# Kernel optimization log

Hardware: AMD Instinct MI355X
Metric: run time of the kernel (lower is better)

Reference implementation:

```python
import jax, jax.numpy as jnp
import numpy as np

E = 1024      # hidden_size
H = 16        # num_attention_heads
HD = E // H   # head_dim
EPS = 1e-5


def _mw_linear(x, Wt, bt, Wi, bi, split):
    # multiway linear: text weights on tokens [:split], image weights on [split:]
    xt = x[:, :split] @ Wt.T + bt
    xi = x[:, split:] @ Wi.T + bi
    return jnp.concatenate([xt, xi], axis=1)


def _ln(x, g, b):
    mu = jnp.mean(x, axis=-1, keepdims=True)
    var = jnp.mean(jnp.square(x - mu), axis=-1, keepdims=True)
    return (x - mu) * jax.lax.rsqrt(var + EPS) * g + b


def _mw_ln(x, gt, bt, gi, bi, split):
    return jnp.concatenate([_ln(x[:, :split], gt, bt), _ln(x[:, split:], gi, bi)], axis=1)


def setup_inputs() -> dict:
    key = jax.random.key(0)
    ks = jax.random.split(key, 24)
    B, T = 8, 1024
    d = {
        'query': jax.random.normal(ks[0], (B, T, E), jnp.float32),
        'key': jax.random.normal(ks[1], (B, T, E), jnp.float32),
        'value': jax.random.normal(ks[2], (B, T, E), jnp.float32),
        'attention_mask': jax.random.normal(ks[3], (T, T), jnp.float32) * 0.02,
    }
    i = 4
    for name in ['q', 'k', 'v', 'o']:
        d[f'W{name}_t'] = jax.random.normal(ks[i], (E, E), jnp.float32) * 0.02; i += 1
        d[f'b{name}_t'] = jnp.zeros((E,), jnp.float32)
        d[f'W{name}_i'] = jax.random.normal(ks[i], (E, E), jnp.float32) * 0.02; i += 1
        d[f'b{name}_i'] = jnp.zeros((E,), jnp.float32)
    d['ln_g_t'] = jnp.ones((E,), jnp.float32)
    d['ln_b_t'] = jnp.zeros((E,), jnp.float32)
    d['ln_g_i'] = jnp.ones((E,), jnp.float32)
    d['ln_b_i'] = jnp.zeros((E,), jnp.float32)
    d['split_position'] = 64
    return d


def reference(query, key, value, attention_mask,
              Wq_t, bq_t, Wq_i, bq_i,
              Wk_t, bk_t, Wk_i, bk_i,
              Wv_t, bv_t, Wv_i, bv_i,
              Wo_t, bo_t, Wo_i, bo_i,
              ln_g_t, ln_b_t, ln_g_i, ln_b_i,
              split_position):
    B, T, _ = query.shape
    S = key.shape[1]
    scaling = HD ** -0.5
    q = _mw_linear(query, Wq_t, bq_t, Wq_i, bq_i, split_position) * scaling
    k = _mw_linear(key, Wk_t, bk_t, Wk_i, bk_i, split_position)
    v = _mw_linear(value, Wv_t, bv_t, Wv_i, bv_i, split_position)
    q = q.reshape(B, T, H, HD)
    k = k.reshape(B, S, H, HD)
    v = v.reshape(B, S, H, HD)
    # [B, H, T, S] attention logits
    attn_weights = jnp.einsum('bthd,bshd->bhts', q, k)
    attn_weights = jnp.nan_to_num(attn_weights) + attention_mask[None, None]
    probs = jax.nn.softmax(attn_weights.astype(jnp.float32), axis=-1).astype(attn_weights.dtype)
    attn = jnp.einsum('bhts,bshd->bthd', probs, v).reshape(B, T, E)
    attn = _mw_ln(attn, ln_g_t, ln_b_t, ln_g_i, ln_b_i, split_position)
    attn = _mw_linear(attn, Wo_t, bo_t, Wo_i, bo_i, split_position)
    return attn
```

## Files before the change

### kernel.cpp

```cpp
#include <hip/hip_runtime.h>

#define E_DIM 1024
#define HEADS 16
#define HD 64

typedef unsigned short ushort_t;
typedef __attribute__((ext_vector_type(8))) short bf16x8;
typedef __attribute__((ext_vector_type(4))) float floatx4;

__device__ inline unsigned int pack2bf(float a, float b) {
    unsigned int ua = __builtin_bit_cast(unsigned int, a);
    unsigned int ub = __builtin_bit_cast(unsigned int, b);
    ua = (ua + 0x8000u) >> 16;
    ub = (ub + 0x8000u) & 0xFFFF0000u;
    return ua | ub;
}
__device__ inline unsigned short f2bf(float a) {
    return (unsigned short)((__builtin_bit_cast(unsigned int, a) + 0x8000u) >> 16);
}
__device__ inline float bf2f(unsigned int s) {
    return __builtin_bit_cast(float, s << 16);
}

__device__ __forceinline__ void load_lds16(const void* g, void* l) {
    __builtin_amdgcn_global_load_lds(
        (const __attribute__((address_space(1))) unsigned int*)g,
        (__attribute__((address_space(3))) unsigned int*)l, 16, 0, 0);
}

__global__ __launch_bounds__(256) void cvt_f32_bf16(
    const float* __restrict__ in, ushort_t* __restrict__ out)
{
    size_t i = ((size_t)blockIdx.x * 256 + threadIdx.x) * 8;
    float4 a = *(const float4*)&in[i];
    float4 b = *(const float4*)&in[i + 4];
    uint4 o;
    o.x = pack2bf(a.x, a.y); o.y = pack2bf(a.z, a.w);
    o.z = pack2bf(b.x, b.y); o.w = pack2bf(b.z, b.w);
    *(uint4*)&out[i] = o;
}

__global__ __launch_bounds__(256) void cvt_weights(
    const float* w0, const float* w1, const float* w2, const float* w3,
    const float* w4, const float* w5, const float* w6, const float* w7,
    ushort_t* __restrict__ out)
{
    const float* srcs[8] = {w0, w1, w2, w3, w4, w5, w6, w7};
    const float* __restrict__ src = srcs[blockIdx.y];
    ushort_t* __restrict__ dst = out + (size_t)blockIdx.y * E_DIM * E_DIM;
    size_t i = ((size_t)blockIdx.x * 256 + threadIdx.x) * 8;
    float4 a = *(const float4*)&src[i];
    float4 b = *(const float4*)&src[i + 4];
    uint4 o;
    o.x = pack2bf(a.x, a.y); o.y = pack2bf(a.z, a.w);
    o.z = pack2bf(b.x, b.y); o.w = pack2bf(b.z, b.w);
    *(uint4*)&dst[i] = o;
}

template<bool OUT_BF16>
__global__ __launch_bounds__(256) void gemm_mw(
    const ushort_t* __restrict__ x,
    const ushort_t* __restrict__ Wt,
    const float* __restrict__ bt,
    const ushort_t* __restrict__ Wi,
    const float* __restrict__ bi,
    void* __restrict__ outv,
    const int* __restrict__ split_ptr,
    float scale, int T_)
{
    const int split = *split_ptr;
    const int kind = blockIdx.z;
    const int m0 = blockIdx.y * 128;
    const int n0 = blockIdx.x * 128;
    const int t0 = m0 % T_;

    if (kind == 0) { if (t0 >= split) return; }
    else           { if (t0 + 128 <= split) return; }

    const ushort_t* __restrict__ W    = (kind == 0) ? Wt : Wi;
    const float*    __restrict__ bias = (kind == 0) ? bt : bi;

    __shared__ __align__(16) ushort_t As[128 * 32];
    __shared__ __align__(16) ushort_t Bs[128 * 32];

    const int tid  = threadIdx.x;
    const int lane = tid & 63;
    const int wv   = tid >> 6;
    const int rw   = (wv >> 1) * 64;
    const int cw   = (wv & 1) * 64;
    const int am   = lane & 15;
    const int aq   = lane >> 4;

    const int grow = wv * 32 + (lane >> 2);
    const int gcol = (lane & 3) * 8;

    floatx4 acc[4][4];
    #pragma unroll
    for (int i = 0; i < 4; ++i)
        #pragma unroll
        for (int j = 0; j < 4; ++j)
            acc[i][j] = (floatx4){0.f, 0.f, 0.f, 0.f};

    for (int k0 = 0; k0 < E_DIM; k0 += 32) {
        load_lds16(&x[(size_t)(m0 + grow) * E_DIM + k0 + gcol],      &As[(wv * 32) * 32]);
        load_lds16(&x[(size_t)(m0 + grow + 16) * E_DIM + k0 + gcol], &As[(wv * 32 + 16) * 32]);
        load_lds16(&W[(size_t)(n0 + grow) * E_DIM + k0 + gcol],      &Bs[(wv * 32) * 32]);
        load_lds16(&W[(size_t)(n0 + grow + 16) * E_DIM + k0 + gcol], &Bs[(wv * 32 + 16) * 32]);
        __syncthreads();

        bf16x8 af[4], bfv[4];
        #pragma unroll
        for (int i = 0; i < 4; ++i)
            af[i] = *(const bf16x8*)&As[(rw + i * 16 + am) * 32 + aq * 8];
        #pragma unroll
        for (int j = 0; j < 4; ++j)
            bfv[j] = *(const bf16x8*)&Bs[(cw + j * 16 + am) * 32 + aq * 8];

        #pragma unroll
        for (int i = 0; i < 4; ++i)
            #pragma unroll
            for (int j = 0; j < 4; ++j)
                acc[i][j] = __builtin_amdgcn_mfma_f32_16x16x32_bf16(af[i], bfv[j], acc[i][j], 0, 0, 0);
        __syncthreads();
    }

    const int cq = lane >> 4;
    const int cm = lane & 15;
    #pragma unroll
    for (int j = 0; j < 4; ++j) {
        int n = n0 + cw + j * 16 + cm;
        float bv = bias[n];
        #pragma unroll
        for (int i = 0; i < 4; ++i) {
            int mbase = m0 + rw + i * 16 + cq * 4;
            #pragma unroll
            for (int r = 0; r < 4; ++r) {
                int m = mbase + r;
                int t = m % T_;
                if (((t < split) ? 0 : 1) != kind) continue;
                float val = (acc[i][j][r] + bv) * scale;
                if (OUT_BF16) ((ushort_t*)outv)[(size_t)m * E_DIM + n] = f2bf(val);
                else          ((float*)outv)[(size_t)m * E_DIM + n] = val;
            }
        }
    }
}

__global__ __launch_bounds__(256) void attn_mfma(
    const ushort_t* __restrict__ q, const ushort_t* __restrict__ k,
    const ushort_t* __restrict__ v, const float* __restrict__ mask,
    ushort_t* __restrict__ outp, int T_)
{
    const int tid  = threadIdx.x;
    const int lane = tid & 63;
    const int wv   = tid >> 6;
    const int h    = blockIdx.y;
    const int b    = blockIdx.z;
    const int r0   = blockIdx.x * 64;

    __shared__ __align__(16) unsigned short Qs[2 * 64 * 40];
    __shared__ __align__(16) unsigned short Ks[2 * 64 * 40];
    __shared__ __align__(16) unsigned short Vst[2 * 64 * 40];
    __shared__ __align__(16) unsigned short Ps[4 * 2 * 16 * 40];

    const int m    = lane & 15;
    const int kq   = lane >> 4;
    const int wrow = wv * 16;

    #pragma unroll
    for (int i = 0; i < 4; ++i) {
        int f   = tid + 256 * i;
        int row = f >> 4;
        int c4  = (f & 15) * 4;
        uint2 a2 = *(const uint2*)&q[((size_t)(b * T_ + r0 + row)) * E_DIM + h * HD + c4];
        int ad = (c4 >> 5) * 2560 + row * 40 + (c4 & 31);
        *(unsigned int*)&Qs[ad]     = a2.x;
        *(unsigned int*)&Qs[ad + 2] = a2.y;
    }
    __syncthreads();

    bf16x8 aq[2];
    aq[0] = *(const bf16x8*)&Qs[0 * 2560 + (wrow + m) * 40 + kq * 8];
    aq[1] = *(const bf16x8*)&Qs[1 * 2560 + (wrow + m) * 40 + kq * 8];

    floatx4 oa[4];
    #pragma unroll
    for (int j = 0; j < 4; ++j) oa[j] = (floatx4){0.f, 0.f, 0.f, 0.f};
    float mrun[4] = {-3.0e38f, -3.0e38f, -3.0e38f, -3.0e38f};
    float lsum[4] = {0.f, 0.f, 0.f, 0.f};

    const int vs0 = (tid >> 4) * 4;
    const int vd0 = (tid & 15) * 4;

    #pragma unroll 1
    for (int s0 = 0; s0 < T_; s0 += 64) {
        __syncthreads();

        #pragma unroll
        for (int i = 0; i < 4; ++i) {
            int f   = tid + 256 * i;
            int row = f >> 4;
            int c4  = (f & 15) * 4;
            uint2 a2 = *(const uint2*)&k[((size_t)(b * T_ + s0 + row)) * E_DIM + h * HD + c4];
            int ad = (c4 >> 5) * 2560 + row * 40 + (c4 & 31);
            *(unsigned int*)&Ks[ad]     = a2.x;
            *(unsigned int*)&Ks[ad + 2] = a2.y;
        }

        {
            uint2 vvr[4];
            #pragma unroll
            for (int i = 0; i < 4; ++i)
                vvr[i] = *(const uint2*)&v[((size_t)(b * T_ + s0 + vs0 + i)) * E_DIM + h * HD + vd0];
            const ushort_t* vp = (const ushort_t*)vvr;
            int plane = (vs0 >> 5) * 2560;
            int sin   = vs0 & 31;
            #pragma unroll
            for (int t = 0; t < 4; ++t) {
                int d  = vd0 + t;
                int pr = d ^ ((d >> 4) & 3);
                uint2 w;
                w.x = (unsigned int)vp[0 * 4 + t] | ((unsigned int)vp[1 * 4 + t] << 16);
                w.y = (unsigned int)vp[2 * 4 + t] | ((unsigned int)vp[3 * 4 + t] << 16);
                *(uint2*)&Vst[plane + pr * 40 + sin] = w;
            }
        }

        float mv[4][4];
        {
            const float* mbase = &mask[(size_t)(r0 + wrow + kq * 4) * T_ + s0 + m];
            #pragma unroll
            for (int j = 0; j < 4; ++j)
                #pragma unroll
                for (int r = 0; r < 4; ++r)
                    mv[j][r] = mbase[r * T_ + j * 16];
        }

        __syncthreads();

        floatx4 sa[4];
        #pragma unroll
        for (int j = 0; j < 4; ++j) sa[j] = (floatx4){0.f, 0.f, 0.f, 0.f};
        #pragma unroll
        for (int c = 0; c < 2; ++c) {
            #pragma unroll
            for (int j = 0; j < 4; ++j) {
                bf16x8 bk = *(const bf16x8*)&Ks[c * 2560 + (j * 16 + m) * 40 + kq * 8];
                sa[j] = __builtin_amdgcn_mfma_f32_16x16x32_bf16(aq[c], bk, sa[j], 0, 0, 0);
            }
        }

        float mnew[4], alpha[4];
        #pragma unroll
        for (int r = 0; r < 4; ++r) {
            sa[0][r] += mv[0][r]; sa[1][r] += mv[1][r];
            sa[2][r] += mv[2][r]; sa[3][r] += mv[3][r];
            float mt = fmaxf(fmaxf(sa[0][r], sa[1][r]), fmaxf(sa[2][r], sa[3][r]));
            mt = fmaxf(mt, __shfl_xor(mt, 1));
            mt = fmaxf(mt, __shfl_xor(mt, 2));
            mt = fmaxf(mt, __shfl_xor(mt, 4));
            mt = fmaxf(mt, __shfl_xor(mt, 8));
            float mn = fmaxf(mrun[r], mt);
            alpha[r] = __expf(mrun[r] - mn);
            mnew[r] = mn;
            mrun[r] = mn;
        }
        #pragma unroll
        for (int j = 0; j < 4; ++j)
            #pragma unroll
            for (int r = 0; r < 4; ++r)
                oa[j][r] *= alpha[r];

        float rs[4] = {0.f, 0.f, 0.f, 0.f};
        #pragma unroll
        for (int j = 0; j < 4; ++j) {
            int gl = ((((j & 1) << 1) | (m >> 3)) ^ kq) & 3;
            int pbase = wv * 1280 + (j >> 1) * 640 + (kq * 4) * 40 + gl * 8 + (m & 7);
            #pragma unroll
            for (int r = 0; r < 4; ++r) {
                float p = __expf(sa[j][r] - mnew[r]);
                rs[r] += p;
                Ps[pbase + r * 40] = f2bf(p);
            }
        }
        #pragma unroll
        for (int r = 0; r < 4; ++r) {
            float s = rs[r];
            s += __shfl_xor(s, 1); s += __shfl_xor(s, 2);
            s += __shfl_xor(s, 4); s += __shfl_xor(s, 8);
            lsum[r] = lsum[r] * alpha[r] + s;
        }

        #pragma unroll
        for (int c = 0; c < 2; ++c) {
            bf16x8 ap = *(const bf16x8*)&Ps[wv * 1280 + c * 640 + m * 40 + ((kq ^ (m >> 2)) & 3) * 8];
            #pragma unroll
            for (int j = 0; j < 4; ++j) {
                int pr = 16 * j + (m ^ j);
                bf16x8 bv = *(const bf16x8*)&Vst[c * 2560 + pr * 40 + kq * 8];
                oa[j] = __builtin_amdgcn_mfma_f32_16x16x32_bf16(ap, bv, oa[j], 0, 0, 0);
            }
        }
    }

    #pragma unroll
    for (int r = 0; r < 4; ++r) {
        float inv = 1.0f / lsum[r];
        size_t orow = ((size_t)(b * T_ + r0 + wrow + kq * 4 + r)) * E_DIM + h * HD;
        #pragma unroll
        for (int j = 0; j < 4; ++j)
            outp[orow + j * 16 + m] = f2bf(oa[j][r] * inv);
    }
}

__global__ __launch_bounds__(256) void mw_ln_bf16(
    const ushort_t* __restrict__ x,
    const float* __restrict__ gt, const float* __restrict__ bt,
    const float* __restrict__ gi, const float* __restrict__ bi,
    ushort_t* __restrict__ out,
    const int* __restrict__ split_ptr, int T_)
{
    const int split = *split_ptr;
    const int row = blockIdx.x;
    const int t = row % T_;
    const float* __restrict__ g  = (t < split) ? gt : gi;
    const float* __restrict__ bb = (t < split) ? bt : bi;

    const int tid = threadIdx.x;
    const int lane = tid & 63;
    const int wid = tid >> 6;

    __shared__ float red[8];

    uint2 xv = *(const uint2*)&x[(size_t)row * E_DIM + tid * 4];
    float f0 = bf2f(xv.x & 0xffffu), f1 = bf2f(xv.x >> 16);
    float f2 = bf2f(xv.y & 0xffffu), f3 = bf2f(xv.y >> 16);
    float s = f0 + f1 + f2 + f3;
    #pragma unroll
    for (int off = 1; off < 64; off <<= 1) s += __shfl_xor(s, off, 64);
    if (lane == 0) red[wid] = s;
    __syncthreads();
    float mu = (red[0] + red[1] + red[2] + red[3]) * (1.0f / E_DIM);

    float d0 = f0 - mu, d1 = f1 - mu, d2 = f2 - mu, d3 = f3 - mu;
    float s2 = d0*d0 + d1*d1 + d2*d2 + d3*d3;
    #pragma unroll
    for (int off = 1; off < 64; off <<= 1) s2 += __shfl_xor(s2, off, 64);
    if (lane == 0) red[4 + wid] = s2;
    __syncthreads();
    float var = (red[4] + red[5] + red[6] + red[7]) * (1.0f / E_DIM);
    float rstd = rsqrtf(var + 1e-5f);

    float4 gv = *(const float4*)&g[tid * 4];
    float4 bv = *(const float4*)&bb[tid * 4];
    uint2 ov;
    ov.x = pack2bf(d0 * rstd * gv.x + bv.x, d1 * rstd * gv.y + bv.y);
    ov.y = pack2bf(d2 * rstd * gv.z + bv.z, d3 * rstd * gv.w + bv.w);
    *(uint2*)&out[(size_t)row * E_DIM + tid * 4] = ov;
}

extern "C" void kernel_launch(void* const* d_in, const int* in_sizes, int n_in,
                              void* d_out, int out_size, void* d_ws, size_t ws_size,
                              hipStream_t stream) {
    const float* query = (const float*)d_in[0];
    const float* key   = (const float*)d_in[1];
    const float* value = (const float*)d_in[2];
    const float* mask  = (const float*)d_in[3];
    const float* Wq_t = (const float*)d_in[4];  const float* bq_t = (const float*)d_in[5];
    const float* Wq_i = (const float*)d_in[6];  const float* bq_i = (const float*)d_in[7];
    const float* Wk_t = (const float*)d_in[8];  const float* bk_t = (const float*)d_in[9];
    const float* Wk_i = (const float*)d_in[10]; const float* bk_i = (const float*)d_in[11];
    const float* Wv_t = (const float*)d_in[12]; const float* bv_t = (const float*)d_in[13];
    const float* Wv_i = (const float*)d_in[14]; const float* bv_i = (const float*)d_in[15];
    const float* Wo_t = (const float*)d_in[16]; const float* bo_t = (const float*)d_in[17];
    const float* Wo_i = (const float*)d_in[18]; const float* bo_i = (const float*)d_in[19];
    const float* ln_g_t = (const float*)d_in[20]; const float* ln_b_t = (const float*)d_in[21];
    const float* ln_g_i = (const float*)d_in[22]; const float* ln_b_i = (const float*)d_in[23];
    const int* split = (const int*)d_in[24];

    float* out = (float*)d_out;

    const int BT = in_sizes[0] / E_DIM;
    const int T_ = 1024;
    const int B  = BT / T_;

    ushort_t* ws = (ushort_t*)d_ws;
    const size_t nx = (size_t)BT * E_DIM;
    const size_t nw = (size_t)E_DIM * E_DIM;
    ushort_t* x_bf = ws;
    ushort_t* q_bf = ws + nx;
    ushort_t* k_bf = ws + 2 * nx;
    ushort_t* v_bf = ws + 3 * nx;
    ushort_t* w_bf = ws + 4 * nx;

    dim3 blk(256);
    dim3 ggrid(E_DIM / 128, BT / 128, 2);
    dim3 agrid(T_ / 64, HEADS, B);
    const int cvt_blocks = (int)(nx / 2048);
    const int wcvt_blocks = (int)(nw / 2048);
    const float scaling = 0.125f;

    cvt_weights<<<dim3(wcvt_blocks, 8), blk, 0, stream>>>(
        Wq_t, Wq_i, Wk_t, Wk_i, Wv_t, Wv_i, Wo_t, Wo_i, w_bf);

    cvt_f32_bf16<<<cvt_blocks, blk, 0, stream>>>(query, x_bf);
    gemm_mw<true><<<ggrid, blk, 0, stream>>>(x_bf, w_bf + 0 * nw, bq_t, w_bf + 1 * nw, bq_i,
                                             q_bf, split, scaling, T_);
    cvt_f32_bf16<<<cvt_blocks, blk, 0, stream>>>(key, x_bf);
    gemm_mw<true><<<ggrid, blk, 0, stream>>>(x_bf, w_bf + 2 * nw, bk_t, w_bf + 3 * nw, bk_i,
                                             k_bf, split, 1.0f, T_);
    cvt_f32_bf16<<<cvt_blocks, blk, 0, stream>>>(value, x_bf);
    gemm_mw<true><<<ggrid, blk, 0, stream>>>(x_bf, w_bf + 4 * nw, bv_t, w_bf + 5 * nw, bv_i,
                                             v_bf, split, 1.0f, T_);

    attn_mfma<<<agrid, blk, 0, stream>>>(q_bf, k_bf, v_bf, mask, q_bf, T_);

    mw_ln_bf16<<<dim3(BT), blk, 0, stream>>>(q_bf, ln_g_t, ln_b_t, ln_g_i, ln_b_i, x_bf, split, T_);

    gemm_mw<false><<<ggrid, blk, 0, stream>>>(x_bf, w_bf + 6 * nw, bo_t, w_bf + 7 * nw, bo_i,
                                              out, split, 1.0f, T_);
}
```

Baseline: 524.0 us.

## Batch QKV projections into one launch and widen attention query tile

The three input conversions now run as a single launch, and the three QKV multiway GEMMs run as one 6-slice grid through a shared GEMM core. The attention kernel now handles 128 query rows per block, two 64-row sub-tiles per wave, so each K/V tile loaded into LDS serves twice as many queries. This cuts launch count and halves K/V global and LDS-staging traffic. In exchange it raises register pressure, halves the attention grid, uses an extra workspace buffer, and places the bf16 Q buffer in the output allocation.

After: 503.2 us. -4.0%, faster.

```diff
diff --git a/kernel.cpp b/kernel.cpp
--- a/kernel.cpp
+++ b/kernel.cpp
@@ -28,16 +28,19 @@
         (__attribute__((address_space(3))) unsigned int*)l, 16, 0, 0);
 }
 
-__global__ __launch_bounds__(256) void cvt_f32_bf16(
-    const float* __restrict__ in, ushort_t* __restrict__ out)
-{
+__global__ __launch_bounds__(256) void cvt_inputs(
+    const float* s0, const float* s1, const float* s2,
+    ushort_t* d0, ushort_t* d1, ushort_t* d2)
+{
+    const float* __restrict__ src = (blockIdx.y == 0) ? s0 : (blockIdx.y == 1) ? s1 : s2;
+    ushort_t* __restrict__ dst = (blockIdx.y == 0) ? d0 : (blockIdx.y == 1) ? d1 : d2;
     size_t i = ((size_t)blockIdx.x * 256 + threadIdx.x) * 8;
-    float4 a = *(const float4*)&in[i];
-    float4 b = *(const float4*)&in[i + 4];
+    float4 a = *(const float4*)&src[i];
+    float4 b = *(const float4*)&src[i + 4];
     uint4 o;
     o.x = pack2bf(a.x, a.y); o.y = pack2bf(a.z, a.w);
     o.z = pack2bf(b.x, b.y); o.w = pack2bf(b.z, b.w);
-    *(uint4*)&out[i] = o;
+    *(uint4*)&dst[i] = o;
 }
 
 __global__ __launch_bounds__(256) void cvt_weights(
@@ -58,28 +61,11 @@
 }
 
 template<bool OUT_BF16>
-__global__ __launch_bounds__(256) void gemm_mw(
-    const ushort_t* __restrict__ x,
-    const ushort_t* __restrict__ Wt,
-    const float* __restrict__ bt,
-    const ushort_t* __restrict__ Wi,
-    const float* __restrict__ bi,
-    void* __restrict__ outv,
-    const int* __restrict__ split_ptr,
-    float scale, int T_)
-{
-    const int split = *split_ptr;
-    const int kind = blockIdx.z;
-    const int m0 = blockIdx.y * 128;
-    const int n0 = blockIdx.x * 128;
-    const int t0 = m0 % T_;
-
-    if (kind == 0) { if (t0 >= split) return; }
-    else           { if (t0 + 128 <= split) return; }
-
-    const ushort_t* __restrict__ W    = (kind == 0) ? Wt : Wi;
-    const float*    __restrict__ bias = (kind == 0) ? bt : bi;
-
+__device__ __forceinline__ void gemm_core(
+    const ushort_t* __restrict__ x, const ushort_t* __restrict__ W,
+    const float* __restrict__ bias, void* __restrict__ outv,
+    int m0, int n0, int split, int kind, float scale, int T_)
+{
     __shared__ __align__(16) ushort_t As[128 * 32];
     __shared__ __align__(16) ushort_t Bs[128 * 32];
 
@@ -146,7 +132,54 @@
     }
 }
 
-__global__ __launch_bounds__(256) void attn_mfma(
+__global__ __launch_bounds__(256) void gemm_qkv(
+    const ushort_t* __restrict__ xq, const ushort_t* __restrict__ xk,
+    const ushort_t* __restrict__ xv, const ushort_t* __restrict__ wall,
+    const float* bq_t, const float* bq_i, const float* bk_t, const float* bk_i,
+    const float* bv_t, const float* bv_i,
+    ushort_t* oq, ushort_t* ok, ushort_t* ov,
+    const int* __restrict__ split_ptr, int T_)
+{
+    const int split = *split_ptr;
+    const int z = blockIdx.z;
+    const int op = z >> 1;
+    const int kind = z & 1;
+    const int m0 = blockIdx.y * 128;
+    const int n0 = blockIdx.x * 128;
+    const int t0 = m0 % T_;
+
+    if (kind == 0) { if (t0 >= split) return; }
+    else           { if (t0 + 128 <= split) return; }
+
+    const ushort_t* x = (op == 0) ? xq : (op == 1) ? xk : xv;
+    ushort_t* outp    = (op == 0) ? oq : (op == 1) ? ok : ov;
+    const ushort_t* W = wall + (size_t)z * E_DIM * E_DIM;
+    const float* bias = (op == 0) ? (kind ? bq_i : bq_t)
+                      : (op == 1) ? (kind ? bk_i : bk_t)
+                                  : (kind ? bv_i : bv_t);
+    float scale = (op == 0) ? 0.125f : 1.0f;
+
+    gemm_core<true>(x, W, bias, outp, m0, n0, split, kind, scale, T_);
+}
+
+__global__ __launch_bounds__(256) void gemm_o(
+    const ushort_t* __restrict__ x, const ushort_t* __restrict__ Wt,
+    const float* bt, const ushort_t* __restrict__ Wi, const float* bi,
+    float* __restrict__ outp, const int* __restrict__ split_ptr, int T_)
+{
+    const int split = *split_ptr;
+    const int kind = blockIdx.z;
+    const int m0 = blockIdx.y * 128;
+    const int n0 = blockIdx.x * 128;
+    const int t0 = m0 % T_;
+
+    if (kind == 0) { if (t0 >= split) return; }
+    else           { if (t0 + 128 <= split) return; }
+
+    gemm_core<false>(x, kind ? Wi : Wt, kind ? bi : bt, outp, m0, n0, split, kind, 1.0f, T_);
+}
+
+__global__ __launch_bounds__(256) void attn_mfma2(
     const ushort_t* __restrict__ q, const ushort_t* __restrict__ k,
     const ushort_t* __restrict__ v, const float* __restrict__ mask,
     ushort_t* __restrict__ outp, int T_)
@@ -156,9 +189,9 @@
     const int wv   = tid >> 6;
     const int h    = blockIdx.y;
     const int b    = blockIdx.z;
-    const int r0   = blockIdx.x * 64;
-
-    __shared__ __align__(16) unsigned short Qs[2 * 64 * 40];
+    const int r0   = blockIdx.x * 128;
+
+    __shared__ __align__(16) unsigned short Qs[2 * 128 * 40];
     __shared__ __align__(16) unsigned short Ks[2 * 64 * 40];
     __shared__ __align__(16) unsigned short Vst[2 * 64 * 40];
     __shared__ __align__(16) unsigned short Ps[4 * 2 * 16 * 40];
@@ -168,26 +201,33 @@
     const int wrow = wv * 16;
 
     #pragma unroll
-    for (int i = 0; i < 4; ++i) {
+    for (int i = 0; i < 8; ++i) {
         int f   = tid + 256 * i;
         int row = f >> 4;
         int c4  = (f & 15) * 4;
         uint2 a2 = *(const uint2*)&q[((size_t)(b * T_ + r0 + row)) * E_DIM + h * HD + c4];
-        int ad = (c4 >> 5) * 2560 + row * 40 + (c4 & 31);
+        int ad = (c4 >> 5) * 5120 + row * 40 + (c4 & 31);
         *(unsigned int*)&Qs[ad]     = a2.x;
         *(unsigned int*)&Qs[ad + 2] = a2.y;
     }
     __syncthreads();
 
-    bf16x8 aq[2];
-    aq[0] = *(const bf16x8*)&Qs[0 * 2560 + (wrow + m) * 40 + kq * 8];
-    aq[1] = *(const bf16x8*)&Qs[1 * 2560 + (wrow + m) * 40 + kq * 8];
-
-    floatx4 oa[4];
-    #pragma unroll
-    for (int j = 0; j < 4; ++j) oa[j] = (floatx4){0.f, 0.f, 0.f, 0.f};
-    float mrun[4] = {-3.0e38f, -3.0e38f, -3.0e38f, -3.0e38f};
-    float lsum[4] = {0.f, 0.f, 0.f, 0.f};
+    bf16x8 aq[2][2];
+    #pragma unroll
+    for (int qs = 0; qs < 2; ++qs)
+        #pragma unroll
+        for (int c = 0; c < 2; ++c)
+            aq[qs][c] = *(const bf16x8*)&Qs[c * 5120 + (qs * 64 + wrow + m) * 40 + kq * 8];
+
+    floatx4 oa[2][4];
+    float mrun[2][4], lsum[2][4];
+    #pragma unroll
+    for (int qs = 0; qs < 2; ++qs)
+        #pragma unroll
+        for (int j = 0; j < 4; ++j) {
+            oa[qs][j] = (floatx4){0.f, 0.f, 0.f, 0.f};
+            mrun[qs][j] = -3.0e38f; lsum[qs][j] = 0.f;
+        }
 
     const int vs0 = (tid >> 4) * 4;
     const int vd0 = (tid & 15) * 4;
@@ -226,91 +266,96 @@
             }
         }
 
-        float mv[4][4];
-        {
-            const float* mbase = &mask[(size_t)(r0 + wrow + kq * 4) * T_ + s0 + m];
+        __syncthreads();
+
+        #pragma unroll
+        for (int qs = 0; qs < 2; ++qs) {
+            float mv[4][4];
+            {
+                const float* mbase = &mask[(size_t)(r0 + qs * 64 + wrow + kq * 4) * T_ + s0 + m];
+                #pragma unroll
+                for (int j = 0; j < 4; ++j)
+                    #pragma unroll
+                    for (int r = 0; r < 4; ++r)
+                        mv[j][r] = mbase[r * T_ + j * 16];
+            }
+
+            floatx4 sa[4];
+            #pragma unroll
+            for (int j = 0; j < 4; ++j) sa[j] = (floatx4){0.f, 0.f, 0.f, 0.f};
+            #pragma unroll
+            for (int c = 0; c < 2; ++c) {
+                #pragma unroll
+                for (int j = 0; j < 4; ++j) {
+                    bf16x8 bk = *(const bf16x8*)&Ks[c * 2560 + (j * 16 + m) * 40 + kq * 8];
+                    sa[j] = __builtin_amdgcn_mfma_f32_16x16x32_bf16(aq[qs][c], bk, sa[j], 0, 0, 0);
+                }
+            }
+
+            float mnew[4], alpha[4];
+            #pragma unroll
+            for (int r = 0; r < 4; ++r) {
+                sa[0][r] += mv[0][r]; sa[1][r] += mv[1][r];
+                sa[2][r] += mv[2][r]; sa[3][r] += mv[3][r];
+                float mt = fmaxf(fmaxf(sa[0][r], sa[1][r]), fmaxf(sa[2][r], sa[3][r]));
+                mt = fmaxf(mt, __shfl_xor(mt, 1));
+                mt = fmaxf(mt, __shfl_xor(mt, 2));
+                mt = fmaxf(mt, __shfl_xor(mt, 4));
+                mt = fmaxf(mt, __shfl_xor(mt, 8));
+                float mn = fmaxf(mrun[qs][r], mt);
+                alpha[r] = __expf(mrun[qs][r] - mn);
+                mnew[r] = mn;
+                mrun[qs][r] = mn;
+            }
             #pragma unroll
             for (int j = 0; j < 4; ++j)
                 #pragma unroll
                 for (int r = 0; r < 4; ++r)
-                    mv[j][r] = mbase[r * T_ + j * 16];
-        }
-
-        __syncthreads();
-
-        floatx4 sa[4];
-        #pragma unroll
-        for (int j = 0; j < 4; ++j) sa[j] = (floatx4){0.f, 0.f, 0.f, 0.f};
-        #pragma unroll
-        for (int c = 0; c < 2; ++c) {
+                    oa[qs][j][r] *= alpha[r];
+
+            float rs[4] = {0.f, 0.f, 0.f, 0.f};
             #pragma unroll
             for (int j = 0; j < 4; ++j) {
-                bf16x8 bk = *(const bf16x8*)&Ks[c * 2560 + (j * 16 + m) * 40 + kq * 8];
-                sa[j] = __builtin_amdgcn_mfma_f32_16x16x32_bf16(aq[c], bk, sa[j], 0, 0, 0);
-            }
-        }
-
-        float mnew[4], alpha[4];
+                int gl = ((((j & 1) << 1) | (m >> 3)) ^ kq) & 3;
+                int pbase = wv * 1280 + (j >> 1) * 640 + (kq * 4) * 40 + gl * 8 + (m & 7);
+                #pragma unroll
+                for (int r = 0; r < 4; ++r) {
+                    float p = __expf(sa[j][r] - mnew[r]);
+                    rs[r] += p;
+                    Ps[pbase + r * 40] = f2bf(p);
+                }
+            }
+            #pragma unroll
+            for (int r = 0; r < 4; ++r) {
+                float s = rs[r];
+                s += __shfl_xor(s, 1); s += __shfl_xor(s, 2);
+                s += __shfl_xor(s, 4); s += __shfl_xor(s, 8);
+                lsum[qs][r] = lsum[qs][r] * alpha[r] + s;
+            }
+
+            #pragma unroll
+            for (int c = 0; c < 2; ++c) {
+                bf16x8 ap = *(const bf16x8*)&Ps[wv * 1280 + c * 640 + m * 40 + ((kq ^ (m >> 2)) & 3) * 8];
+                #pragma unroll
+                for (int j = 0; j < 4; ++j) {
+                    int pr = 16 * j + (m ^ j);
+                    bf16x8 bv = *(const bf16x8*)&Vst[c * 2560 + pr * 40 + kq * 8];
+                    oa[qs][j] = __builtin_amdgcn_mfma_f32_16x16x32_bf16(ap, bv, oa[qs][j], 0, 0, 0);
+                }
+            }
+        }
+    }
+
+    #pragma unroll
+    for (int qs = 0; qs < 2; ++qs)
         #pragma unroll
         for (int r = 0; r < 4; ++r) {
-            sa[0][r] += mv[0][r]; sa[1][r] += mv[1][r];
-            sa[2][r] += mv[2][r]; sa[3][r] += mv[3][r];
-            float mt = fmaxf(fmaxf(sa[0][r], sa[1][r]), fmaxf(sa[2][r], sa[3][r]));
-            mt = fmaxf(mt, __shfl_xor(mt, 1));
-            mt = fmaxf(mt, __shfl_xor(mt, 2));
-            mt = fmaxf(mt, __shfl_xor(mt, 4));
-            mt = fmaxf(mt, __shfl_xor(mt, 8));
-            float mn = fmaxf(mrun[r], mt);
-            alpha[r] = __expf(mrun[r] - mn);
-            mnew[r] = mn;
-            mrun[r] = mn;
-        }
-        #pragma unroll
-        for (int j = 0; j < 4; ++j)
-            #pragma unroll
-            for (int r = 0; r < 4; ++r)
-                oa[j][r] *= alpha[r];
-
-        float rs[4] = {0.f, 0.f, 0.f, 0.f};
-        #pragma unroll
-        for (int j = 0; j < 4; ++j) {
-            int gl = ((((j & 1) << 1) | (m >> 3)) ^ kq) & 3;
-            int pbase = wv * 1280 + (j >> 1) * 640 + (kq * 4) * 40 + gl * 8 + (m & 7);
-            #pragma unroll
-            for (int r = 0; r < 4; ++r) {
-                float p = __expf(sa[j][r] - mnew[r]);
-                rs[r] += p;
-                Ps[pbase + r * 40] = f2bf(p);
-            }
-        }
-        #pragma unroll
-        for (int r = 0; r < 4; ++r) {
-            float s = rs[r];
-            s += __shfl_xor(s, 1); s += __shfl_xor(s, 2);
-            s += __shfl_xor(s, 4); s += __shfl_xor(s, 8);
-            lsum[r] = lsum[r] * alpha[r] + s;
-        }
-
-        #pragma unroll
-        for (int c = 0; c < 2; ++c) {
-            bf16x8 ap = *(const bf16x8*)&Ps[wv * 1280 + c * 640 + m * 40 + ((kq ^ (m >> 2)) & 3) * 8];
-            #pragma unroll
-            for (int j = 0; j < 4; ++j) {
-                int pr = 16 * j + (m ^ j);
-                bf16x8 bv = *(const bf16x8*)&Vst[c * 2560 + pr * 40 + kq * 8];
-                oa[j] = __builtin_amdgcn_mfma_f32_16x16x32_bf16(ap, bv, oa[j], 0, 0, 0);
-            }
-        }
-    }
-
-    #pragma unroll
-    for (int r = 0; r < 4; ++r) {
-        float inv = 1.0f / lsum[r];
-        size_t orow = ((size_t)(b * T_ + r0 + wrow + kq * 4 + r)) * E_DIM + h * HD;
-        #pragma unroll
-        for (int j = 0; j < 4; ++j)
-            outp[orow + j * 16 + m] = f2bf(oa[j][r] * inv);
-    }
+            float inv = 1.0f / lsum[qs][r];
+            size_t orow = ((size_t)(b * T_ + r0 + qs * 64 + wrow + kq * 4 + r)) * E_DIM + h * HD;
+            #pragma unroll
+            for (int j = 0; j < 4; ++j)
+                outp[orow + j * 16 + m] = f2bf(oa[qs][j][r] * inv);
+        }
 }
 
 __global__ __launch_bounds__(256) void mw_ln_bf16(
@@ -387,36 +432,34 @@
     ushort_t* ws = (ushort_t*)d_ws;
     const size_t nx = (size_t)BT * E_DIM;
     const size_t nw = (size_t)E_DIM * E_DIM;
-    ushort_t* x_bf = ws;
-    ushort_t* q_bf = ws + nx;
-    ushort_t* k_bf = ws + 2 * nx;
-    ushort_t* v_bf = ws + 3 * nx;
-    ushort_t* w_bf = ws + 4 * nx;
+    ushort_t* xq_bf = ws;
+    ushort_t* xk_bf = ws + nx;
+    ushort_t* xv_bf = ws + 2 * nx;
+    ushort_t* k_bf  = ws + 3 * nx;
+    ushort_t* v_bf  = ws + 4 * nx;
+    ushort_t* w_bf  = ws + 5 * nx;
+    ushort_t* q_bf  = (ushort_t*)d_out;
 
     dim3 blk(256);
-    dim3 ggrid(E_DIM / 128, BT / 128, 2);
-    dim3 agrid(T_ / 64, HEADS, B);
     const int cvt_blocks = (int)(nx / 2048);
     const int wcvt_blocks = (int)(nw / 2048);
-    const float scaling = 0.125f;
 
     cvt_weights<<<dim3(wcvt_blocks, 8), blk, 0, stream>>>(
         Wq_t, Wq_i, Wk_t, Wk_i, Wv_t, Wv_i, Wo_t, Wo_i, w_bf);
-
-    cvt_f32_bf16<<<cvt_blocks, blk, 0, stream>>>(query, x_bf);
-    gemm_mw<true><<<ggrid, blk, 0, stream>>>(x_bf, w_bf + 0 * nw, bq_t, w_bf + 1 * nw, bq_i,
-                                             q_bf, split, scaling, T_);
-    cvt_f32_bf16<<<cvt_blocks, blk, 0, stream>>>(key, x_bf);
-    gemm_mw<true><<<ggrid, blk, 0, stream>>>(x_bf, w_bf + 2 * nw, bk_t, w_bf + 3 * nw, bk_i,
-                                             k_bf, split, 1.0f, T_);
-    cvt_f32_bf16<<<cvt_blocks, blk, 0, stream>>>(value, x_bf);
-    gemm_mw<true><<<ggrid, blk, 0, stream>>>(x_bf, w_bf + 4 * nw, bv_t, w_bf + 5 * nw, bv_i,
-                                             v_bf, split, 1.0f, T_);
-
-    attn_mfma<<<agrid, blk, 0, stream>>>(q_bf, k_bf, v_bf, mask, q_bf, T_);
-
-    mw_ln_bf16<<<dim3(BT), blk, 0, stream>>>(q_bf, ln_g_t, ln_b_t, ln_g_i, ln_b_i, x_bf, split, T_);
-
-    gemm_mw<false><<<ggrid, blk, 0, stream>>>(x_bf, w_bf + 6 * nw, bo_t, w_bf + 7 * nw, bo_i,
-                                              out, split, 1.0f, T_);
-}
+    cvt_inputs<<<dim3(cvt_blocks, 3), blk, 0, stream>>>(
+        query, key, value, xq_bf, xk_bf, xv_bf);
+
+    gemm_qkv<<<dim3(E_DIM / 128, BT / 128, 6), blk, 0, stream>>>(
+        xq_bf, xk_bf, xv_bf, w_bf,
+        bq_t, bq_i, bk_t, bk_i, bv_t, bv_i,
+        q_bf, k_bf, v_bf, split, T_);
+
+    attn_mfma2<<<dim3(T_ / 128, HEADS, B), blk, 0, stream>>>(
+        q_bf, k_bf, v_bf, mask, q_bf, T_);
+
+    mw_ln_bf16<<<dim3(BT), blk, 0, stream>>>(
+        q_bf, ln_g_t, ln_b_t, ln_g_i, ln_b_i, xq_bf, split, T_);
+
+    gemm_o<<<dim3(E_DIM / 128, BT / 128, 2), blk, 0, stream>>>(
+        xq_bf, w_bf + 6 * nw, bo_t, w_bf + 7 * nw, bo_i, out, split, T_);
+}
```
